# Kernel optimization log

Hardware: AMD Instinct MI355X
Metric: run time of the kernel (lower is better)

The kernel has to match this reference:

```python
import jax, jax.numpy as jnp
import numpy as np

B, S, E, H = 2, 2048, 2048, 16
D = E // H  # head_dim = 128


def rotate_half(x):
    x1, x2 = jnp.split(x, 2, axis=-1)
    return jnp.concatenate([-x2, x1], axis=-1)


def rope_sincos(seq_len, dim):
    inv_freq = 1.0 / (10000.0 ** (jnp.arange(0, dim, 2, dtype=jnp.float32) / dim))
    t = jnp.arange(seq_len, dtype=jnp.float32)
    freqs = jnp.outer(t, inv_freq)            # [S, D/2]
    emb = jnp.concatenate([freqs, freqs], -1)  # [S, D]
    return jnp.sin(emb), jnp.cos(emb)


def apply_rope(x, sin, cos):
    # x: [B, S, H, D]; sin/cos: [S, D] -> [1, S, 1, D]
    sin = sin[None, :, None, :]
    cos = cos[None, :, None, :]
    return x * cos + rotate_half(x) * sin


def setup_inputs() -> dict:
    key = jax.random.key(0)
    k1, k2 = jax.random.split(key)
    x = jax.random.normal(k1, (B, S, E), dtype=jnp.float32)
    # causal boolean mask [B, 1, S, S]
    mask = jnp.broadcast_to(jnp.tril(jnp.ones((S, S), dtype=bool))[None, None], (B, 1, S, S))
    # fused QKV projection weight (hk.Linear, no bias): [E, 3E]
    W_qkv = jax.random.normal(k2, (E, 3 * E), dtype=jnp.float32) / np.sqrt(E)
    return {"x": x, "mask": mask, "W_qkv": W_qkv}


def reference(x, mask, W_qkv):
    seq_len = x.shape[1]
    qkv = x @ W_qkv                               # [B, S, 3E]
    q, k, v = jnp.split(qkv, 3, axis=-1)
    q = q.reshape(-1, seq_len, H, D)
    k = k.reshape(-1, seq_len, H, D)
    v = v.reshape(-1, seq_len, H, D)
    sin, cos = rope_sincos(seq_len, D)
    q = apply_rope(q, sin, cos)
    k = apply_rope(k, sin, cos)
    attn = jnp.einsum('bqhd,bkhd->bhqk', q, k) / jnp.sqrt(jnp.float32(D))
    m = jnp.broadcast_to(mask, (mask.shape[0], H, seq_len, k.shape[1]))
    attn = jnp.where(m, attn, -jnp.inf)
    attn = jax.nn.softmax(attn, axis=-1)
    out = jnp.einsum('bhqk,bkhd->bqhd', attn, v)
    return out.reshape(-1, seq_len, H * D)
```

## Files before the change

kernel.cpp:

```cpp
#include <hip/hip_runtime.h>

typedef __bf16 bf16;
typedef __bf16 bf16x8 __attribute__((ext_vector_type(8)));
typedef __bf16 bf16x4 __attribute__((ext_vector_type(4)));
typedef float f32x4 __attribute__((ext_vector_type(4)));

#define MFMA16(a, b, c) __builtin_amdgcn_mfma_f32_16x16x32_bf16(a, b, c, 0, 0, 0)

#define Bq 2
#define Sq 2048
#define Eq 2048
#define Hq 16
#define Dq 128
#define N3E 6144

#define KSC (0.08838834764831845f * 1.4426950408889634f)

#define GLOAD_LDS16(gp, lp) \
  __builtin_amdgcn_global_load_lds( \
      (const __attribute__((address_space(1))) void*)(gp), \
      (__attribute__((address_space(3))) void*)(lp), 16, 0, 0)

__device__ __forceinline__ bf16 f2bf(float f) {
  unsigned u = __builtin_bit_cast(unsigned, f);
  u += 0x7FFFu + ((u >> 16) & 1u);
  unsigned short h = (unsigned short)(u >> 16);
  return __builtin_bit_cast(bf16, h);
}
__device__ __forceinline__ float bf2f(bf16 b) {
  unsigned short h = __builtin_bit_cast(unsigned short, b);
  return __builtin_bit_cast(float, (unsigned)h << 16);
}

__global__ __launch_bounds__(256) void prep(const float* __restrict__ x,
                                            bf16* __restrict__ xb,
                                            const float* __restrict__ w,
                                            bf16* __restrict__ wt,
                                            float2* __restrict__ tbl) {
  __shared__ __align__(16) bf16 T[64][72];
  const int tid = threadIdx.x;
  const int bidx = blockIdx.x;

  if (bidx < 2048) {
    const size_t i = ((size_t)bidx * 256 + tid) * 16;
#pragma unroll
    for (int hh = 0; hh < 2; ++hh) {
      float4 a = *(const float4*)(x + i + hh * 8);
      float4 b = *(const float4*)(x + i + hh * 8 + 4);
      bf16x8 o;
      o[0] = f2bf(a.x); o[1] = f2bf(a.y); o[2] = f2bf(a.z); o[3] = f2bf(a.w);
      o[4] = f2bf(b.x); o[5] = f2bf(b.y); o[6] = f2bf(b.z); o[7] = f2bf(b.w);
      *(bf16x8*)(xb + i + hh * 8) = o;
    }
  } else if (bidx < 2048 + 3072) {
    const int b2 = bidx - 2048;
    const int kb = b2 & 31;
    const int nb = b2 >> 5;
    const int k0 = kb * 64, n0 = nb * 64;
    {
      const int kr = tid >> 4, nc = (tid & 15) * 4;
#pragma unroll
      for (int p = 0; p < 4; ++p) {
        const int k = kr + p * 16;
        float4 v = *(const float4*)(w + (size_t)(k0 + k) * N3E + n0 + nc);
        T[nc + 0][k] = f2bf(v.x);
        T[nc + 1][k] = f2bf(v.y);
        T[nc + 2][k] = f2bf(v.z);
        T[nc + 3][k] = f2bf(v.w);
      }
    }
    __syncthreads();
#pragma unroll
    for (int q = 0; q < 2; ++q) {
      const int id = q * 256 + tid;
      const int n = id >> 3, ch = id & 7;
      bf16x8 v = *(const bf16x8*)&T[n][ch * 8];
      *(bf16x8*)(wt + (size_t)(n0 + n) * Eq + k0 + ch * 8) = v;
    }
  } else {
    const int i = (bidx - 5120) * 256 + tid;
    const int s = i >> 6, d = i & 63;
    const float freq = __expf(-(float)d * 0.14391157f);
    const float ang = (float)s * freq;
    float sv, cv;
    __sincosf(ang, &sv, &cv);
    tbl[i] = make_float2(cv, sv);
  }
}

__global__ __launch_bounds__(512, 2) void gemm_qkv(
    const bf16* __restrict__ xb, const bf16* __restrict__ wt,
    const float2* __restrict__ tbl, bf16* __restrict__ qws,
    bf16* __restrict__ kws, bf16* __restrict__ vtws) {
  __shared__ __align__(16) bf16 LDS[3 * 24576];

  const int tid = threadIdx.x;
  const int lane = tid & 63, wv = tid >> 6;
  const int q4 = lane >> 4, c = lane & 15;
  const int wm = (wv >> 2) * 64;
  const int wn = (wv & 3) * 64;
  const int cx = c & 7;

  const int bid = blockIdx.x;
  const int wg = (bid & 7) * 96 + (bid >> 3);
  const int m0 = (wg & 31) * 128;
  const int n0 = (wg >> 5) * 256;

  f32x4 acc[4][4];
#pragma unroll
  for (int i = 0; i < 4; ++i)
#pragma unroll
    for (int j = 0; j < 4; ++j) acc[i][j] = {0.f, 0.f, 0.f, 0.f};

  const int NT = Eq / 64;

  auto stage = [&](int t, int st) {
    bf16* ab = LDS + st * 24576;
    bf16* bb = ab + 8192;
    const int k0 = t * 64;
#pragma unroll
    for (int it = 0; it < 2; ++it) {
      const int slot = it * 512 + tid;
      const int row = slot >> 3, kch = slot & 7;
      const int kcs = kch ^ (row & 7);
      GLOAD_LDS16(xb + (size_t)(m0 + row) * Eq + k0 + kcs * 8, ab + slot * 8);
    }
#pragma unroll
    for (int it = 0; it < 4; ++it) {
      const int slot = it * 512 + tid;
      const int row = slot >> 3, kch = slot & 7;
      const int kcs = kch ^ (row & 7);
      GLOAD_LDS16(wt + (size_t)(n0 + row) * Eq + k0 + kcs * 8, bb + slot * 8);
    }
  };

  stage(0, 0);
  stage(1, 1);
  asm volatile("s_waitcnt vmcnt(6)" ::: "memory");
  __builtin_amdgcn_s_barrier();

  int stC = 0;
#pragma unroll 1
  for (int t = 0; t < NT; ++t) {
    if (t + 2 < NT) {
      int ss = stC + 2;
      if (ss >= 3) ss -= 3;
      stage(t + 2, ss);
    }
    const bf16* A = LDS + stC * 24576;
    const bf16* Bb = A + 8192;
#pragma unroll
    for (int kk = 0; kk < 64; kk += 32) {
      const int bch = kk >> 3;
      bf16x8 af[4], bfr[4];
#pragma unroll
      for (int i = 0; i < 4; ++i)
        af[i] = *(const bf16x8*)
            &A[(wm + i * 16 + c) * 64 + ((bch + q4) ^ cx) * 8];
#pragma unroll
      for (int j = 0; j < 4; ++j)
        bfr[j] = *(const bf16x8*)
            &Bb[(wn + j * 16 + c) * 64 + ((bch + q4) ^ cx) * 8];
      __builtin_amdgcn_s_setprio(1);
#pragma unroll
      for (int i = 0; i < 4; ++i)
#pragma unroll
        for (int j = 0; j < 4; ++j)
          acc[i][j] = MFMA16(af[i], bfr[j], acc[i][j]);
      __builtin_amdgcn_s_setprio(0);
    }
    if (t + 1 < NT) {
      if (t + 2 < NT) asm volatile("s_waitcnt vmcnt(6)" ::: "memory");
      else            asm volatile("s_waitcnt vmcnt(0)" ::: "memory");
      __builtin_amdgcn_s_barrier();
    }
    stC = stC == 2 ? 0 : stC + 1;
  }
  __syncthreads();

  const int t3 = n0 >> 11;
  const int b = m0 >> 11;
  const int s0 = m0 & 2047;
  const int h0 = (n0 & 2047) >> 7;

  bf16* E = LDS;

  if (t3 == 2) {
#pragma unroll 1
    for (int hh = 0; hh < 2; ++hh) {
      if (((wv & 3) >> 1) == hh) {
#pragma unroll
        for (int i = 0; i < 4; ++i)
#pragma unroll
          for (int j = 0; j < 4; ++j) {
            bf16x4 pv;
            pv[0] = f2bf(acc[i][j][0]); pv[1] = f2bf(acc[i][j][1]);
            pv[2] = f2bf(acc[i][j][2]); pv[3] = f2bf(acc[i][j][3]);
            *(bf16x4*)&E[((wn & 127) + j * 16 + c) * 136 + wm + i * 16 +
                         q4 * 4] = pv;
          }
      }
      __syncthreads();
      bf16* vbase = vtws + ((size_t)(b * Hq + h0 + hh) * Dq) * Sq + s0;
#pragma unroll
      for (int p = 0; p < 4; ++p) {
        const int id = p * 512 + tid;
        const int d = id >> 4, ch = id & 15;
        bf16x8 v = *(const bf16x8*)&E[d * 136 + ch * 8];
        *(bf16x8*)&vbase[(size_t)d * Sq + ch * 8] = v;
      }
      __syncthreads();
    }
  } else {
    const float qs = (t3 == 0) ? (float)KSC : 1.0f;
#pragma unroll 1
    for (int hh = 0; hh < 2; ++hh) {
      if (((wv & 3) >> 1) == hh) {
#pragma unroll
        for (int i = 0; i < 4; ++i)
#pragma unroll
          for (int j = 0; j < 4; ++j)
#pragma unroll
            for (int rr = 0; rr < 4; ++rr)
              E[(wm + i * 16 + q4 * 4 + rr) * 136 + (wn & 127) + j * 16 + c] =
                  f2bf(acc[i][j][rr]);
      }
      __syncthreads();
      bf16* hd = ((t3 == 0) ? qws : kws) +
                 ((size_t)(b * Hq + h0 + hh) * Sq + s0) * Dq;
#pragma unroll
      for (int p = 0; p < 2; ++p) {
        const int row = p * 64 + (tid >> 3);
        const int dlow = (tid & 7) * 8;
        const int s = s0 + row;
        bf16x8 lo = *(const bf16x8*)&E[row * 136 + dlow];
        bf16x8 hi = *(const bf16x8*)&E[row * 136 + 64 + dlow];
        const float2* tb = tbl + (size_t)s * 64 + dlow;
        bf16x8 olo, ohi;
#pragma unroll
        for (int e = 0; e < 8; ++e) {
          const float cv = tb[e].x, sv = tb[e].y;
          const float x1 = bf2f(lo[e]), x2 = bf2f(hi[e]);
          olo[e] = f2bf((x1 * cv - x2 * sv) * qs);
          ohi[e] = f2bf((x2 * cv + x1 * sv) * qs);
        }
        *(bf16x8*)&hd[(size_t)row * Dq + dlow] = olo;
        *(bf16x8*)&hd[(size_t)row * Dq + 64 + dlow] = ohi;
      }
      __syncthreads();
    }
  }
}

__device__ const int dSQT0[16] = {15,15, 7,14,14, 6,13,13,12,12,11,11, 8,10,10, 9};
__device__ const int dSSP0[16] = { 0, 1, 2, 0, 1, 2, 0, 1, 0, 1, 0, 1, 0, 0, 1, 0};
__device__ const int dSQT1[16] = {-1,-1,-1,-1,-1,-1,-1,-1, 0, 1, 2, 3, 5, 8, 4, 9};
__device__ const int dSSP1[16] = { 0, 0, 0, 0, 0, 0, 0, 0, 2, 2, 2, 2, 2, 1, 2, 1};
__device__ const int dZP[16]   = { 9, 2, 1,13,15,12,14,11,10, 0, 8, 7, 5, 3, 6, 4};

__global__ __launch_bounds__(256, 2) void attn_kernel(
    const bf16* __restrict__ qws, const bf16* __restrict__ kws,
    const bf16* __restrict__ vtws, float* __restrict__ out,
    float* __restrict__ opart, float* __restrict__ ml) {
  __shared__ __align__(16) bf16 Kld[2][8192];
  __shared__ __align__(16) bf16 Vld[2][8192];
  __shared__ __align__(16) bf16 Plds[4][16][72];

  const int tid = threadIdx.x, lane = tid & 63, wave = tid >> 6;
  const int q4 = lane >> 4, c = lane & 15;
  const int h = blockIdx.y, b = blockIdx.z;
  const int sidx = (b == 0) ? blockIdx.x : dZP[blockIdx.x];

  const size_t bh = (size_t)(b * Hq + h);
  const bf16* qbase = qws + bh * Sq * Dq;
  const bf16* kbase = kws + bh * Sq * Dq;
  const bf16* vbase = vtws + bh * Dq * Sq;

#pragma unroll 1
  for (int seg = 0; seg < 2; ++seg) {
    const int qt = (seg == 0) ? dSQT0[sidx] : dSQT1[sidx];
    if (qt < 0) break;
    const int sp = (seg == 0) ? dSSP0[sidx] : dSSP1[sidx];
    const bool split = (sp != 2);
    const int c0 = split ? sp * (qt + 1) : 0;
    const int c1 = split ? c0 + (qt + 1) : 2 * qt + 2;
    const int q0 = qt * 128 + wave * 32;

    bf16x8 qf[2][4];
#pragma unroll
    for (int g = 0; g < 2; ++g)
#pragma unroll
      for (int ks = 0; ks < 4; ++ks)
        qf[g][ks] = *(const bf16x8*)
            &qbase[(size_t)(q0 + g * 16 + c) * Dq + ks * 32 + q4 * 8];

    f32x4 Ot[2][8];
    float m_i[2], l_i[2];
#pragma unroll
    for (int g = 0; g < 2; ++g) {
#pragma unroll
      for (int dj = 0; dj < 8; ++dj) Ot[g][dj] = {0.f, 0.f, 0.f, 0.f};
      m_i[g] = -1e30f; l_i[g] = 0.f;
    }

    __syncthreads();
    {
      const int koff0 = c0 * 64;
#pragma unroll
      for (int it = 0; it < 4; ++it) {
        const int slot = it * 256 + tid;
        GLOAD_LDS16(
            kbase + (size_t)(koff0 + (slot & 63)) * Dq + (slot >> 6) * 8,
            &Kld[c0 & 1][slot * 8]);
        GLOAD_LDS16(
            vbase + (size_t)(slot & 127) * Sq + koff0 + (slot >> 7) * 8,
            &Vld[c0 & 1][slot * 8]);
      }
    }

    for (int kb = c0; kb < c1; ++kb) {
      const int buf = kb & 1;
      asm volatile("s_waitcnt vmcnt(0)" ::: "memory");
      __builtin_amdgcn_s_barrier();
      if (kb + 1 < c1) {
        const int nb = buf ^ 1;
        const int koff = (kb + 1) * 64;
#pragma unroll
        for (int it = 0; it < 4; ++it) {
          const int slot = it * 256 + tid;
          GLOAD_LDS16(
              kbase + (size_t)(koff + (slot & 63)) * Dq + (slot >> 6) * 8,
              &Kld[nb][slot * 8]);
          GLOAD_LDS16(
              vbase + (size_t)(slot & 127) * Sq + koff + (slot >> 7) * 8,
              &Vld[nb][slot * 8]);
        }
      }
      const bool masked = (kb >= 2 * qt);
#pragma unroll
      for (int g = 0; g < 2; ++g) {
        const int qg = q0 + g * 16 + c;
        f32x4 st[4];
#pragma unroll
        for (int j8 = 0; j8 < 4; ++j8) st[j8] = {0.f, 0.f, 0.f, 0.f};
        __builtin_amdgcn_s_setprio(1);
#pragma unroll
        for (int ks = 0; ks < 4; ++ks) {
          const bf16x8 qv = qf[g][ks];
#pragma unroll
          for (int j8 = 0; j8 < 4; ++j8) {
            const bf16x8 kv = *(const bf16x8*)
                &Kld[buf][((ks * 4 + q4) * 64 + j8 * 16 + c) * 8];
            st[j8] = MFMA16(kv, qv, st[j8]);
          }
        }
        __builtin_amdgcn_s_setprio(0);
        if (masked) {
          const int kb64 = kb * 64 + q4 * 4;
#pragma unroll
          for (int j8 = 0; j8 < 4; ++j8)
#pragma unroll
            for (int rr = 0; rr < 4; ++rr)
              if (kb64 + j8 * 16 + rr > qg) st[j8][rr] = -1e30f;
        }
        float mloc = -1e30f;
#pragma unroll
        for (int j8 = 0; j8 < 4; ++j8)
#pragma unroll
          for (int rr = 0; rr < 4; ++rr) mloc = fmaxf(mloc, st[j8][rr]);
        mloc = fmaxf(mloc, __shfl_xor(mloc, 16, 64));
        mloc = fmaxf(mloc, __shfl_xor(mloc, 32, 64));
        float mn = m_i[g];
        if (__any(mloc > mn)) {
          mn = fmaxf(mn, mloc);
          const float alpha = exp2f(m_i[g] - mn);
          m_i[g] = mn;
          l_i[g] *= alpha;
#pragma unroll
          for (int dj = 0; dj < 8; ++dj) Ot[g][dj] *= alpha;
        }
        float ssum = 0.f;
#pragma unroll
        for (int j8 = 0; j8 < 4; ++j8)
#pragma unroll
          for (int rr = 0; rr < 4; ++rr) {
            const float p = exp2f(st[j8][rr] - mn);
            st[j8][rr] = p;
            ssum += p;
          }
        ssum += __shfl_xor(ssum, 16, 64);
        ssum += __shfl_xor(ssum, 32, 64);
        l_i[g] += ssum;
#pragma unroll
        for (int j8 = 0; j8 < 4; ++j8) {
          bf16x4 pk;
          pk[0] = f2bf(st[j8][0]); pk[1] = f2bf(st[j8][1]);
          pk[2] = f2bf(st[j8][2]); pk[3] = f2bf(st[j8][3]);
          *(bf16x4*)&Plds[wave][c][j8 * 16 + q4 * 4] = pk;
        }
        __builtin_amdgcn_s_setprio(1);
#pragma unroll
        for (int ks = 0; ks < 2; ++ks) {
          const bf16x8 pv = *(const bf16x8*)&Plds[wave][c][ks * 32 + q4 * 8];
#pragma unroll
          for (int dj = 0; dj < 8; ++dj) {
            const bf16x8 vv = *(const bf16x8*)
                &Vld[buf][((ks * 4 + q4) * 128 + dj * 16 + c) * 8];
            Ot[g][dj] = MFMA16(vv, pv, Ot[g][dj]);
          }
        }
        __builtin_amdgcn_s_setprio(0);
      }
    }

    if (!split) {
#pragma unroll
      for (int g = 0; g < 2; ++g) {
        const float inv = 1.0f / l_i[g];
        float* orow = out + ((size_t)b * Sq + q0 + g * 16 + c) * Eq + h * Dq;
#pragma unroll
        for (int dj = 0; dj < 8; ++dj) {
          float4 o;
          o.x = Ot[g][dj][0] * inv; o.y = Ot[g][dj][1] * inv;
          o.z = Ot[g][dj][2] * inv; o.w = Ot[g][dj][3] * inv;
          *(float4*)&orow[dj * 16 + q4 * 4] = o;
        }
      }
    } else {
      const int tix = (((b * Hq + h) * 8) + (qt - 8)) * 2 + sp;
#pragma unroll
      for (int g = 0; g < 2; ++g) {
        const int wrow = wave * 32 + g * 16 + c;
        float* prow = opart + ((size_t)tix * 128 + wrow) * 128;
#pragma unroll
        for (int dj = 0; dj < 8; ++dj) {
          float4 o;
          o.x = Ot[g][dj][0]; o.y = Ot[g][dj][1];
          o.z = Ot[g][dj][2]; o.w = Ot[g][dj][3];
          *(float4*)&prow[dj * 16 + q4 * 4] = o;
        }
        if (q4 == 0) {
          ml[((size_t)tix * 128 + wrow) * 2 + 0] = m_i[g];
          ml[((size_t)tix * 128 + wrow) * 2 + 1] = l_i[g];
        }
      }
    }
  }
}

__global__ __launch_bounds__(256) void attn_combine(
    const float* __restrict__ opart, const float* __restrict__ ml,
    float* __restrict__ out) {
  const int tile = blockIdx.x;
  const int qt = (tile & 7) + 8;
  const int hb = tile >> 3;
  const int h = hb & 15, b = hb >> 4;
  const int tid = threadIdx.x;
  const int r = tid >> 1;
  const int d0 = (tid & 1) * 64;
  const int t0 = tile * 2, t1 = t0 + 1;

  const float m0 = ml[((size_t)t0 * 128 + r) * 2 + 0];
  const float l0 = ml[((size_t)t0 * 128 + r) * 2 + 1];
  const float m1 = ml[((size_t)t1 * 128 + r) * 2 + 0];
  const float l1 = ml[((size_t)t1 * 128 + r) * 2 + 1];
  const float m = fmaxf(m0, m1);
  const float w0 = exp2f(m0 - m);
  const float w1 = exp2f(m1 - m);
  const float inv = 1.0f / (l0 * w0 + l1 * w1);
  const float s0 = w0 * inv, s1 = w1 * inv;

  const float* p0 = opart + ((size_t)t0 * 128 + r) * 128 + d0;
  const float* p1 = opart + ((size_t)t1 * 128 + r) * 128 + d0;
  float* orow = out + ((size_t)(b * Sq + qt * 128 + r)) * Eq + h * Dq + d0;
#pragma unroll
  for (int i = 0; i < 16; ++i) {
    float4 a = *(const float4*)&p0[i * 4];
    float4 bb = *(const float4*)&p1[i * 4];
    float4 o;
    o.x = a.x * s0 + bb.x * s1;
    o.y = a.y * s0 + bb.y * s1;
    o.z = a.z * s0 + bb.z * s1;
    o.w = a.w * s0 + bb.w * s1;
    *(float4*)&orow[i * 4] = o;
  }
}

extern "C" void kernel_launch(void* const* d_in, const int* in_sizes, int n_in,
                              void* d_out, int out_size, void* d_ws,
                              size_t ws_size, hipStream_t stream) {
  const float* x = (const float*)d_in[0];
  const float* w = (const float*)d_in[2];
  float* out = (float*)d_out;

  const size_t nX = (size_t)Bq * Sq * Eq;
  const size_t nW = (size_t)Eq * N3E;
  const size_t perT = (size_t)Bq * Hq * Sq * Dq;

  bf16* xb = (bf16*)d_ws;
  bf16* wt = xb + nX;
  bf16* qws = wt + nW;
  bf16* kws = qws + perT;
  bf16* vtws = kws + perT;
  float2* tbl = (float2*)(vtws + perT);
  float* wsend = (float*)(tbl + (size_t)Sq * 64);

  const size_t nOpart = (size_t)512 * 128 * 128;
  const size_t nMl = (size_t)512 * 128 * 2;
  const size_t usedB = (size_t)((char*)wsend - (char*)d_ws);
  float* opart;
  if (ws_size >= usedB + (nOpart + nMl) * sizeof(float)) {
    opart = wsend;
  } else {
    opart = (float*)d_ws;
  }
  float* ml = opart + nOpart;

  prep<<<5632, 256, 0, stream>>>(x, xb, w, wt, tbl);

  gemm_qkv<<<768, 512, 0, stream>>>(xb, wt, tbl, qws, kws, vtws);

  dim3 g3(16, 16, 2);
  attn_kernel<<<g3, 256, 0, stream>>>(qws, kws, vtws, out, opart, ml);

  attn_combine<<<256, 256, 0, stream>>>(opart, ml, out);
}
```

Before: 361.7 us.

## Single-buffer K/V LDS tiles in attention to fit three blocks per CU

Drops the double-buffered K/V shared-memory tiles for single buffers and raises the launch bound from 2 to 3 blocks per multiprocessor. The next tile's load is now issued after all waves finish the current tile, behind an added barrier. This gives up load/compute overlap inside a block and relies on the extra resident blocks to hide global-load latency. Per-block LDS falls from roughly 73KB to about 41KB, and the higher occupancy target may tighten the register budget and cause spills.

```diff
diff --git a/kernel.cpp b/kernel.cpp
--- a/kernel.cpp
+++ b/kernel.cpp
@@ -258,12 +258,12 @@
 __device__ const int dSSP1[16] = { 0, 0, 0, 0, 0, 0, 0, 0, 2, 2, 2, 2, 2, 1, 2, 1};
 __device__ const int dZP[16]   = { 9, 2, 1,13,15,12,14,11,10, 0, 8, 7, 5, 3, 6, 4};
 
-__global__ __launch_bounds__(256, 2) void attn_kernel(
+__global__ __launch_bounds__(256, 3) void attn_kernel(
     const bf16* __restrict__ qws, const bf16* __restrict__ kws,
     const bf16* __restrict__ vtws, float* __restrict__ out,
     float* __restrict__ opart, float* __restrict__ ml) {
-  __shared__ __align__(16) bf16 Kld[2][8192];
-  __shared__ __align__(16) bf16 Vld[2][8192];
+  __shared__ __align__(16) bf16 Kld[8192];
+  __shared__ __align__(16) bf16 Vld[8192];
   __shared__ __align__(16) bf16 Plds[4][16][72];
 
   const int tid = threadIdx.x, lane = tid & 63, wave = tid >> 6;
@@ -275,6 +275,18 @@
   const bf16* qbase = qws + bh * Sq * Dq;
   const bf16* kbase = kws + bh * Sq * Dq;
   const bf16* vbase = vtws + bh * Dq * Sq;
+
+  auto stageKV = [&](int kb) {
+    const int koff = kb * 64;
+#pragma unroll
+    for (int it = 0; it < 4; ++it) {
+      const int slot = it * 256 + tid;
+      GLOAD_LDS16(kbase + (size_t)(koff + (slot & 63)) * Dq + (slot >> 6) * 8,
+                  &Kld[slot * 8]);
+      GLOAD_LDS16(vbase + (size_t)(slot & 127) * Sq + koff + (slot >> 7) * 8,
+                  &Vld[slot * 8]);
+    }
+  };
 
 #pragma unroll 1
   for (int seg = 0; seg < 2; ++seg) {
@@ -304,38 +316,11 @@
     }
 
     __syncthreads();
-    {
-      const int koff0 = c0 * 64;
-#pragma unroll
-      for (int it = 0; it < 4; ++it) {
-        const int slot = it * 256 + tid;
-        GLOAD_LDS16(
-            kbase + (size_t)(koff0 + (slot & 63)) * Dq + (slot >> 6) * 8,
-            &Kld[c0 & 1][slot * 8]);
-        GLOAD_LDS16(
-            vbase + (size_t)(slot & 127) * Sq + koff0 + (slot >> 7) * 8,
-            &Vld[c0 & 1][slot * 8]);
-      }
-    }
+    stageKV(c0);
 
     for (int kb = c0; kb < c1; ++kb) {
-      const int buf = kb & 1;
       asm volatile("s_waitcnt vmcnt(0)" ::: "memory");
       __builtin_amdgcn_s_barrier();
-      if (kb + 1 < c1) {
-        const int nb = buf ^ 1;
-        const int koff = (kb + 1) * 64;
-#pragma unroll
-        for (int it = 0; it < 4; ++it) {
-          const int slot = it * 256 + tid;
-          GLOAD_LDS16(
-              kbase + (size_t)(koff + (slot & 63)) * Dq + (slot >> 6) * 8,
-              &Kld[nb][slot * 8]);
-          GLOAD_LDS16(
-              vbase + (size_t)(slot & 127) * Sq + koff + (slot >> 7) * 8,
-              &Vld[nb][slot * 8]);
-        }
-      }
       const bool masked = (kb >= 2 * qt);
 #pragma unroll
       for (int g = 0; g < 2; ++g) {
@@ -350,7 +335,7 @@
 #pragma unroll
           for (int j8 = 0; j8 < 4; ++j8) {
             const bf16x8 kv = *(const bf16x8*)
-                &Kld[buf][((ks * 4 + q4) * 64 + j8 * 16 + c) * 8];
+                &Kld[((ks * 4 + q4) * 64 + j8 * 16 + c) * 8];
             st[j8] = MFMA16(kv, qv, st[j8]);
           }
         }
@@ -405,12 +390,14 @@
 #pragma unroll
           for (int dj = 0; dj < 8; ++dj) {
             const bf16x8 vv = *(const bf16x8*)
-                &Vld[buf][((ks * 4 + q4) * 128 + dj * 16 + c) * 8];
+                &Vld[((ks * 4 + q4) * 128 + dj * 16 + c) * 8];
             Ot[g][dj] = MFMA16(vv, pv, Ot[g][dj]);
           }
         }
         __builtin_amdgcn_s_setprio(0);
       }
+      __builtin_amdgcn_s_barrier();
+      if (kb + 1 < c1) stageKV(kb + 1);
     }
 
     if (!split) {
```

New measurement: 386.5 us. 6.8% more time.

## Shrink QKV GEMM tile to 128x128 and drop triple-buffered LDS pipeline

Applied to the files above, without the earlier changes.

The QKV GEMM moves from 512-thread blocks with 128x256 tiles and a three-stage global-to-LDS prefetch pipeline to 256-thread blocks with 128x128 tiles and a single LDS buffer. Each k-step now loads, waits for all loads and computes, and the grid doubles to 1536 blocks. The epilogue drops its two-pass per-head loop because a tile now covers exactly one head. This cuts LDS use per block, which may let more blocks share a CU, but it gives up overlap of loads with MFMA work and doubles operand reloads per output.

```diff
diff --git a/kernel.cpp b/kernel.cpp
--- a/kernel.cpp
+++ b/kernel.cpp
@@ -88,23 +88,25 @@
   }
 }
 
-__global__ __launch_bounds__(512, 2) void gemm_qkv(
+__global__ __launch_bounds__(256) void gemm_qkv(
     const bf16* __restrict__ xb, const bf16* __restrict__ wt,
     const float2* __restrict__ tbl, bf16* __restrict__ qws,
     bf16* __restrict__ kws, bf16* __restrict__ vtws) {
-  __shared__ __align__(16) bf16 LDS[3 * 24576];
+  __shared__ __align__(16) bf16 Sm[17408];
+  bf16* Ald = Sm;
+  bf16* Bld = Sm + 8192;
 
   const int tid = threadIdx.x;
   const int lane = tid & 63, wv = tid >> 6;
   const int q4 = lane >> 4, c = lane & 15;
-  const int wm = (wv >> 2) * 64;
-  const int wn = (wv & 3) * 64;
+  const int wm = (wv >> 1) * 64;
+  const int wn = (wv & 1) * 64;
   const int cx = c & 7;
 
   const int bid = blockIdx.x;
-  const int wg = (bid & 7) * 96 + (bid >> 3);
+  const int wg = (bid & 7) * 192 + (bid >> 3);
   const int m0 = (wg & 31) * 128;
-  const int n0 = (wg >> 5) * 256;
+  const int n0 = (wg >> 5) * 128;
 
   f32x4 acc[4][4];
 #pragma unroll
@@ -114,41 +116,27 @@
 
   const int NT = Eq / 64;
 
-  auto stage = [&](int t, int st) {
-    bf16* ab = LDS + st * 24576;
-    bf16* bb = ab + 8192;
+#pragma unroll 1
+  for (int t = 0; t < NT; ++t) {
     const int k0 = t * 64;
 #pragma unroll
-    for (int it = 0; it < 2; ++it) {
-      const int slot = it * 512 + tid;
+    for (int it = 0; it < 4; ++it) {
+      const int slot = it * 256 + tid;
       const int row = slot >> 3, kch = slot & 7;
       const int kcs = kch ^ (row & 7);
-      GLOAD_LDS16(xb + (size_t)(m0 + row) * Eq + k0 + kcs * 8, ab + slot * 8);
+      GLOAD_LDS16(xb + (size_t)(m0 + row) * Eq + k0 + kcs * 8,
+                  Ald + slot * 8);
     }
 #pragma unroll
     for (int it = 0; it < 4; ++it) {
-      const int slot = it * 512 + tid;
+      const int slot = it * 256 + tid;
       const int row = slot >> 3, kch = slot & 7;
       const int kcs = kch ^ (row & 7);
-      GLOAD_LDS16(wt + (size_t)(n0 + row) * Eq + k0 + kcs * 8, bb + slot * 8);
-    }
-  };
-
-  stage(0, 0);
-  stage(1, 1);
-  asm volatile("s_waitcnt vmcnt(6)" ::: "memory");
-  __builtin_amdgcn_s_barrier();
-
-  int stC = 0;
-#pragma unroll 1
-  for (int t = 0; t < NT; ++t) {
-    if (t + 2 < NT) {
-      int ss = stC + 2;
-      if (ss >= 3) ss -= 3;
-      stage(t + 2, ss);
-    }
-    const bf16* A = LDS + stC * 24576;
-    const bf16* Bb = A + 8192;
+      GLOAD_LDS16(wt + (size_t)(n0 + row) * Eq + k0 + kcs * 8,
+                  Bld + slot * 8);
+    }
+    asm volatile("s_waitcnt vmcnt(0)" ::: "memory");
+    __builtin_amdgcn_s_barrier();
 #pragma unroll
     for (int kk = 0; kk < 64; kk += 32) {
       const int bch = kk >> 3;
@@ -156,11 +144,11 @@
 #pragma unroll
       for (int i = 0; i < 4; ++i)
         af[i] = *(const bf16x8*)
-            &A[(wm + i * 16 + c) * 64 + ((bch + q4) ^ cx) * 8];
+            &Ald[(wm + i * 16 + c) * 64 + ((bch + q4) ^ cx) * 8];
 #pragma unroll
       for (int j = 0; j < 4; ++j)
         bfr[j] = *(const bf16x8*)
-            &Bb[(wn + j * 16 + c) * 64 + ((bch + q4) ^ cx) * 8];
+            &Bld[(wn + j * 16 + c) * 64 + ((bch + q4) ^ cx) * 8];
       __builtin_amdgcn_s_setprio(1);
 #pragma unroll
       for (int i = 0; i < 4; ++i)
@@ -169,12 +157,7 @@
           acc[i][j] = MFMA16(af[i], bfr[j], acc[i][j]);
       __builtin_amdgcn_s_setprio(0);
     }
-    if (t + 1 < NT) {
-      if (t + 2 < NT) asm volatile("s_waitcnt vmcnt(6)" ::: "memory");
-      else            asm volatile("s_waitcnt vmcnt(0)" ::: "memory");
-      __builtin_amdgcn_s_barrier();
-    }
-    stC = stC == 2 ? 0 : stC + 1;
+    __builtin_amdgcn_s_barrier();
   }
   __syncthreads();
 
@@ -183,71 +166,58 @@
   const int s0 = m0 & 2047;
   const int h0 = (n0 & 2047) >> 7;
 
-  bf16* E = LDS;
+  bf16* E = Sm;
 
   if (t3 == 2) {
-#pragma unroll 1
-    for (int hh = 0; hh < 2; ++hh) {
-      if (((wv & 3) >> 1) == hh) {
-#pragma unroll
-        for (int i = 0; i < 4; ++i)
-#pragma unroll
-          for (int j = 0; j < 4; ++j) {
-            bf16x4 pv;
-            pv[0] = f2bf(acc[i][j][0]); pv[1] = f2bf(acc[i][j][1]);
-            pv[2] = f2bf(acc[i][j][2]); pv[3] = f2bf(acc[i][j][3]);
-            *(bf16x4*)&E[((wn & 127) + j * 16 + c) * 136 + wm + i * 16 +
-                         q4 * 4] = pv;
-          }
-      }
-      __syncthreads();
-      bf16* vbase = vtws + ((size_t)(b * Hq + h0 + hh) * Dq) * Sq + s0;
-#pragma unroll
-      for (int p = 0; p < 4; ++p) {
-        const int id = p * 512 + tid;
-        const int d = id >> 4, ch = id & 15;
-        bf16x8 v = *(const bf16x8*)&E[d * 136 + ch * 8];
-        *(bf16x8*)&vbase[(size_t)d * Sq + ch * 8] = v;
-      }
-      __syncthreads();
+#pragma unroll
+    for (int i = 0; i < 4; ++i)
+#pragma unroll
+      for (int j = 0; j < 4; ++j) {
+        bf16x4 pv;
+        pv[0] = f2bf(acc[i][j][0]); pv[1] = f2bf(acc[i][j][1]);
+        pv[2] = f2bf(acc[i][j][2]); pv[3] = f2bf(acc[i][j][3]);
+        *(bf16x4*)&E[(wn + j * 16 + c) * 136 + wm + i * 16 + q4 * 4] = pv;
+      }
+    __syncthreads();
+    bf16* vbase = vtws + ((size_t)(b * Hq + h0) * Dq) * Sq + s0;
+#pragma unroll
+    for (int p = 0; p < 8; ++p) {
+      const int id = p * 256 + tid;
+      const int d = id >> 4, ch = id & 15;
+      bf16x8 v = *(const bf16x8*)&E[d * 136 + ch * 8];
+      *(bf16x8*)&vbase[(size_t)d * Sq + ch * 8] = v;
     }
   } else {
     const float qs = (t3 == 0) ? (float)KSC : 1.0f;
-#pragma unroll 1
-    for (int hh = 0; hh < 2; ++hh) {
-      if (((wv & 3) >> 1) == hh) {
-#pragma unroll
-        for (int i = 0; i < 4; ++i)
-#pragma unroll
-          for (int j = 0; j < 4; ++j)
-#pragma unroll
-            for (int rr = 0; rr < 4; ++rr)
-              E[(wm + i * 16 + q4 * 4 + rr) * 136 + (wn & 127) + j * 16 + c] =
-                  f2bf(acc[i][j][rr]);
-      }
-      __syncthreads();
-      bf16* hd = ((t3 == 0) ? qws : kws) +
-                 ((size_t)(b * Hq + h0 + hh) * Sq + s0) * Dq;
-#pragma unroll
-      for (int p = 0; p < 2; ++p) {
-        const int row = p * 64 + (tid >> 3);
-        const int dlow = (tid & 7) * 8;
-        const int s = s0 + row;
-        bf16x8 lo = *(const bf16x8*)&E[row * 136 + dlow];
-        bf16x8 hi = *(const bf16x8*)&E[row * 136 + 64 + dlow];
-        const float2* tb = tbl + (size_t)s * 64 + dlow;
-        bf16x8 olo, ohi;
-#pragma unroll
-        for (int e = 0; e < 8; ++e) {
-          const float cv = tb[e].x, sv = tb[e].y;
-          const float x1 = bf2f(lo[e]), x2 = bf2f(hi[e]);
-          olo[e] = f2bf((x1 * cv - x2 * sv) * qs);
-          ohi[e] = f2bf((x2 * cv + x1 * sv) * qs);
-        }
-        *(bf16x8*)&hd[(size_t)row * Dq + dlow] = olo;
-        *(bf16x8*)&hd[(size_t)row * Dq + 64 + dlow] = ohi;
-      }
-      __syncthreads();
+#pragma unroll
+    for (int i = 0; i < 4; ++i)
+#pragma unroll
+      for (int j = 0; j < 4; ++j)
+#pragma unroll
+        for (int rr = 0; rr < 4; ++rr)
+          E[(wm + i * 16 + q4 * 4 + rr) * 136 + wn + j * 16 + c] =
+              f2bf(acc[i][j][rr]);
+    __syncthreads();
+    bf16* hd = ((t3 == 0) ? qws : kws) +
+               ((size_t)(b * Hq + h0) * Sq + s0) * Dq;
+#pragma unroll
+    for (int p = 0; p < 4; ++p) {
+      const int row = p * 32 + (tid >> 3);
+      const int dlow = (tid & 7) * 8;
+      const int s = s0 + row;
+      bf16x8 lo = *(const bf16x8*)&E[row * 136 + dlow];
+      bf16x8 hi = *(const bf16x8*)&E[row * 136 + 64 + dlow];
+      const float2* tb = tbl + (size_t)s * 64 + dlow;
+      bf16x8 olo, ohi;
+#pragma unroll
+      for (int e = 0; e < 8; ++e) {
+        const float cv = tb[e].x, sv = tb[e].y;
+        const float x1 = bf2f(lo[e]), x2 = bf2f(hi[e]);
+        olo[e] = f2bf((x1 * cv - x2 * sv) * qs);
+        ohi[e] = f2bf((x2 * cv + x1 * sv) * qs);
+      }
+      *(bf16x8*)&hd[(size_t)row * Dq + dlow] = olo;
+      *(bf16x8*)&hd[(size_t)row * Dq + 64 + dlow] = ohi;
     }
   }
 }
@@ -518,7 +488,7 @@
 
   prep<<<5632, 256, 0, stream>>>(x, xb, w, wt, tbl);
 
-  gemm_qkv<<<768, 512, 0, stream>>>(xb, wt, tbl, qws, kws, vtws);
+  gemm_qkv<<<1536, 256, 0, stream>>>(xb, wt, tbl, qws, kws, vtws);
 
   dim3 g3(16, 16, 2);
   attn_kernel<<<g3, 256, 0, stream>>>(qws, kws, vtws, out, opart, ml);
```

New measurement: 515.8 us. 1.43x slower.
